# Kernel tuning notes

Measured on AMD Instinct MI355X. Metric: run time of the kernel, lower is better.

## Reference

```python
import jax, jax.numpy as jnp
import numpy as np

DIM = 768
H = 12          # num query heads
KV = 6          # num kv heads
GS = H // KV    # group size = 2
HD = DIM // H   # head dim = 64


def setup_inputs() -> dict:
    key = jax.random.key(0)
    ks = jax.random.split(key, 6)
    B, P = 8, 1024
    s = DIM ** -0.5
    x = jax.random.normal(ks[0], (B, P, DIM), dtype=jnp.float32)
    Wq = jax.random.normal(ks[1], (DIM, DIM), dtype=jnp.float32) * s
    Wk = jax.random.normal(ks[2], (DIM, KV * HD), dtype=jnp.float32) * s
    Wv = jax.random.normal(ks[3], (DIM, KV * HD), dtype=jnp.float32) * s
    Wp = jax.random.normal(ks[4], (DIM, DIM), dtype=jnp.float32) * s
    bp = jnp.zeros((DIM,), dtype=jnp.float32)
    return {"x": x, "Wq": Wq, "Wk": Wk, "Wv": Wv, "Wp": Wp, "bp": bp}


def reference(x, Wq, Wk, Wv, Wp, bp):
    B, P, C = x.shape
    scale = HD ** -0.5
    # projections; consecutive heads i*GS..(i+1)*GS-1 form kv-group i (torch.split dim=1)
    q = (x @ Wq).reshape(B, P, KV, GS, HD).transpose(0, 2, 3, 1, 4) * scale  # [B,KV,GS,P,d]
    k = (x @ Wk).reshape(B, P, KV, HD).transpose(0, 2, 1, 3)                 # [B,KV,P,d]
    v = (x @ Wv).reshape(B, P, KV, HD).transpose(0, 2, 1, 3)                 # [B,KV,P,d]

    scores = jnp.einsum('bghqd,bgkd->bghqk', q, k)      # [B,KV,GS,P,P]
    w = jax.nn.softmax(scores, axis=-1)                  # attn_drop=0 (eval)
    att = jnp.einsum('bghqk,bgkd->bghqd', w, v)          # [B,KV,GS,P,d]

    # per-group row-matched gaussian-ish noise (torch get_gaussian), vectorized over KV groups
    y = P * HD
    flat = att.reshape(B, KV, GS, y)                     # rows = groups within kv-group
    M = jax.random.uniform(jax.random.key(42), (KV, GS, y), dtype=flat.dtype)
    di = jnp.arange(min(GS, y))
    M = M.at[:, di, di].set(0.0)                         # sparse: zero diagonal
    m_mean = M.mean(axis=-1, keepdims=True)
    m_std = jnp.std(M, axis=-1, ddof=1, keepdims=True)   # torch.std is unbiased
    m_std = jnp.where(m_std == 0, jnp.ones_like(m_std), m_std)
    Z = (M - m_mean) / m_std                             # [KV,GS,y], shared across batch
    r_mean = flat.mean(axis=-1, keepdims=True)           # [B,KV,GS,1]
    r_std = jnp.std(flat, axis=-1, ddof=1, keepdims=True)
    flat = flat - (Z[None] * r_std + r_mean)

    att = flat.reshape(B, KV, GS, P, HD).reshape(B, H, P, HD)
    out = att.transpose(0, 2, 1, 3).reshape(B, P, C) @ Wp + bp  # proj_drop=0
    return out
```

## Files before the change

kernel.cpp:

```cpp
#include <hip/hip_runtime.h>
#include <hip/hip_bf16.h>
#include <math.h>


#define NTHREADS 256

typedef __bf16 bf16x8 __attribute__((ext_vector_type(8)));
typedef float f32x4 __attribute__((ext_vector_type(4)));

#define MFMA16(a, b, c) __builtin_amdgcn_mfma_f32_16x16x32_bf16(a, b, c, 0, 0, 0)

#define QSCALE 0.18033688011112042f

__device__ __forceinline__ float fexp2(float x) {
#if __has_builtin(__builtin_amdgcn_exp2f)
    return __builtin_amdgcn_exp2f(x);
#else
    return __expf(x * 0.6931471805599453f);
#endif
}

__device__ __forceinline__ void gload16(const void* g, void* l) {
    __builtin_amdgcn_global_load_lds(
        (const __attribute__((address_space(1))) void*)g,
        (__attribute__((address_space(3))) void*)l, 16, 0, 0);
}

__device__ __forceinline__ unsigned rotl_u32(unsigned x, int r) {
    return (x << r) | (x >> (32 - r));
}
__device__ __forceinline__ void threefry_0_42(unsigned x0, unsigned x1,
                                              unsigned& o0, unsigned& o1) {
    const unsigned ks0 = 0u, ks1 = 42u, ks2 = 0u ^ 42u ^ 0x1BD11BDAu;
    x0 += ks0; x1 += ks1;
#define R4(a,b,c,d) \
    x0 += x1; x1 = rotl_u32(x1,a); x1 ^= x0; \
    x0 += x1; x1 = rotl_u32(x1,b); x1 ^= x0; \
    x0 += x1; x1 = rotl_u32(x1,c); x1 ^= x0; \
    x0 += x1; x1 = rotl_u32(x1,d); x1 ^= x0;
    R4(13,15,26,6)   x0 += ks1; x1 += ks2 + 1u;
    R4(17,29,16,24)  x0 += ks2; x1 += ks0 + 2u;
    R4(13,15,26,6)   x0 += ks0; x1 += ks1 + 3u;
    R4(17,29,16,24)  x0 += ks1; x1 += ks2 + 4u;
    R4(13,15,26,6)   x0 += ks2; x1 += ks0 + 5u;
#undef R4
    o0 = x0; o1 = x1;
}
__device__ __forceinline__ float tf_uniform(unsigned i) {
    unsigned o0, o1;
    threefry_0_42(0u, i, o0, o1);
    unsigned bits = o0 ^ o1;
    return __uint_as_float((bits >> 9) | 0x3f800000u) - 1.0f;
}

__device__ __forceinline__ float wave_sum64(float v) {
#pragma unroll
    for (int off = 32; off; off >>= 1) v += __shfl_xor(v, off, 64);
    return v;
}

__device__ __forceinline__ unsigned short bf16_rne(float x) {
    unsigned u = __float_as_uint(x);
    return (unsigned short)((u + 0x7fffu + ((u >> 16) & 1u)) >> 16);
}
__device__ __forceinline__ unsigned pack_bf16x2(float lo, float hi) {
    unsigned ul = __float_as_uint(lo), uh = __float_as_uint(hi);
    unsigned rl = ul + 0x7fffu + ((ul >> 16) & 1u);
    unsigned rh = uh + 0x7fffu + ((uh >> 16) & 1u);
    return __builtin_amdgcn_perm(rh, rl, 0x07060302u);
}
__device__ __forceinline__ float bfu(unsigned v) {
    return __uint_as_float(v << 16);
}


__global__ __launch_bounds__(NTHREADS) void prep_k(
    const float* __restrict__ x, const float* __restrict__ Wq,
    const float* __restrict__ Wk, const float* __restrict__ Wv,
    const float* __restrict__ Wp,
    unsigned short* __restrict__ xb, unsigned short* __restrict__ wstk,
    unsigned short* __restrict__ wpt,
    unsigned short* __restrict__ zb, float* __restrict__ zpart)
{
    __shared__ float rbuf[8];
    int blk = blockIdx.x;
    if (blk < 1536) {
#pragma unroll
        for (int j = 0; j < 4; ++j) {
            int i = blk * 1024 + j * 256 + threadIdx.x;
            float4 v = ((const float4*)x)[i];
            uint2 u;
            u.x = pack_bf16x2(v.x, v.y);
            u.y = pack_bf16x2(v.z, v.w);
            int f0 = i * 4;
            int row = f0 / 768, col = f0 - row * 768;
            int kc = col >> 6, kin = col & 63;
            int kh = kin >> 5, g = (kin >> 3) & 3, e = col & 7;
            int chunk = row >> 4, cl = row & 15;
            size_t a = (((size_t)(kc * 512 + chunk)) * 2 + kh) * 512
                       + (g * 16 + cl) * 8 + e;
            *(uint2*)&xb[a] = u;
        }
    } else if (blk < 1920) {
        int zc = blk - 1536;
        int row = zc >> 5, chunk = zc & 31;
        int g = row & 1;
        int j0 = chunk * 2048;
        float sum = 0.f, sumsq = 0.f;
        for (int t = threadIdx.x; t < 2048; t += NTHREADS) {
            int j = j0 + t;
            unsigned i = (unsigned)row * 65536u + (unsigned)j;
            float m = tf_uniform(i);
            if (j == g) m = 0.f;
            zb[i] = bf16_rne(m);
            sum += m; sumsq += m * m;
        }
        sum = wave_sum64(sum); sumsq = wave_sum64(sumsq);
        int lane = threadIdx.x & 63, wv = threadIdx.x >> 6;
        if (lane == 0) { rbuf[wv] = sum; rbuf[4 + wv] = sumsq; }
        __syncthreads();
        if (threadIdx.x == 0) {
            zpart[zc * 2]     = rbuf[0] + rbuf[1] + rbuf[2] + rbuf[3];
            zpart[zc * 2 + 1] = rbuf[4] + rbuf[5] + rbuf[6] + rbuf[7];
        }
    } else {
        int id = blk - 1920;
        const float* W; unsigned short* dstbuf; int N, rowbase, NC;
        if (id < 144)      { W = Wq; dstbuf = wstk; N = 768; rowbase = 0;    NC = 96; }
        else if (id < 216) { W = Wk; dstbuf = wstk; N = 384; rowbase = 768;  NC = 96; id -= 144; }
        else if (id < 288) { W = Wv; dstbuf = wstk; N = 384; rowbase = 1152; NC = 96; id -= 216; }
        else               { W = Wp; dstbuf = wpt;  N = 768; rowbase = 0;    NC = 48; id -= 288; }
        int ntn = N >> 6;
        int kt = id / ntn, nt = id % ntn;
        int k0 = kt * 64, n0 = nt * 64;
        int t = threadIdx.x;
        int tn = t & 63, tk = t >> 6;
        float r[16];
#pragma unroll
        for (int j = 0; j < 16; ++j)
            r[j] = W[(size_t)(k0 + tk * 16 + j) * N + n0 + tn];
        uint4 u0, u1;
        u0.x = pack_bf16x2(r[0], r[1]);   u0.y = pack_bf16x2(r[2], r[3]);
        u0.z = pack_bf16x2(r[4], r[5]);   u0.w = pack_bf16x2(r[6], r[7]);
        u1.x = pack_bf16x2(r[8], r[9]);   u1.y = pack_bf16x2(r[10], r[11]);
        u1.z = pack_bf16x2(r[12], r[13]); u1.w = pack_bf16x2(r[14], r[15]);
        int rowg = rowbase + n0 + tn;
        int chunk = rowg >> 4, cl = rowg & 15;
        int kc = k0 >> 6;
        int kh = tk >> 1, g0 = (tk & 1) * 2;
        size_t base = (((size_t)(kc * NC + chunk)) * 2 + kh) * 512 + cl * 8;
        *(uint4*)&dstbuf[base + g0 * 128]       = u0;
        *(uint4*)&dstbuf[base + (g0 + 1) * 128] = u1;
    }
}

__device__ __forceinline__ void mfma_tile128x256(
    const unsigned short* __restrict__ Afb, int nca,
    const unsigned short* __restrict__ Bfb,
    int row0, int col0,
    unsigned short* As, unsigned short* Bs, f32x4 acc[4][4])
{
    const int tid = threadIdx.x;
    const int lane = tid & 63, w = tid >> 6;
    const int c = lane & 15, g = lane >> 4;
    const int wm = w & 1, wn = w >> 1;

#pragma unroll
    for (int mi = 0; mi < 4; ++mi)
#pragma unroll
        for (int ni = 0; ni < 4; ++ni) acc[mi][ni] = (f32x4){0.f, 0.f, 0.f, 0.f};

    const unsigned short* Abase = Afb + (size_t)(row0 >> 4) * 1024;
    const unsigned short* Bbase = Bfb + (size_t)(col0 >> 4) * 1024;

    for (int kc = 0; kc < 12; ++kc) {
        const unsigned short* a = Abase + (size_t)kc * nca * 1024;
        const unsigned short* bb = Bbase + (size_t)kc * 512 * 1024;
        __syncthreads();
        gload16(a  + tid * 8,         As + tid * 8);
        gload16(a  + tid * 8 + 4096,  As + tid * 8 + 4096);
        gload16(bb + tid * 8,         Bs + tid * 8);
        gload16(bb + tid * 8 + 4096,  Bs + tid * 8 + 4096);
        gload16(bb + tid * 8 + 8192,  Bs + tid * 8 + 8192);
        gload16(bb + tid * 8 + 12288, Bs + tid * 8 + 12288);
        __syncthreads();
#pragma unroll
        for (int ks = 0; ks < 2; ++ks) {
            bf16x8 aA[4], bB[4];
#pragma unroll
            for (int mi = 0; mi < 4; ++mi)
                aA[mi] = *(const bf16x8*)&As[(wm * 4 + mi) * 1024 + ks * 512 + g * 128 + c * 8];
#pragma unroll
            for (int ni = 0; ni < 4; ++ni)
                bB[ni] = *(const bf16x8*)&Bs[(wn * 4 + ni) * 1024 + ks * 512 + g * 128 + c * 8];
#pragma unroll
            for (int mi = 0; mi < 4; ++mi)
#pragma unroll
                for (int ni = 0; ni < 4; ++ni)
                    acc[mi][ni] = MFMA16(aA[mi], bB[ni], acc[mi][ni]);
        }
    }
}

__global__ __launch_bounds__(512) void qkv_mfma_k(
    const unsigned short* __restrict__ xb, const unsigned short* __restrict__ wstk,
    unsigned short* __restrict__ qbh, unsigned short* __restrict__ kb2,
    unsigned short* __restrict__ vb2)
{
    __shared__ unsigned short As[8192];
    __shared__ unsigned short Bs[16384];
    int id = blockIdx.x;
    int xcd = id & 7, slot = id >> 3;
    int col0i = xcd + ((slot & 3) << 3);
    int row0i = slot >> 2;
    int row0 = row0i * 128, col0 = col0i * 256;
    f32x4 acc[4][4];
    mfma_tile128x256(wstk, 96, xb, row0, col0, As, Bs, acc);

    const int tid = threadIdx.x;
    const int w = tid >> 6, lane = tid & 63;
    const int c = lane & 15, g = lane >> 4;
    const int wm = w & 1, wn = w >> 1;

#pragma unroll
    for (int mi = 0; mi < 4; ++mi) {
        int ocb = row0 + wm * 64 + mi * 16;
        int ocol = ocb + g * 4;
#pragma unroll
        for (int ni = 0; ni < 4; ++ni) {
            int pglob = col0 + wn * 64 + ni * 16 + c;
            int b = pglob >> 10, pin = pglob & 1023;
            if (ocb < 768) {
                ushort4 u;
                u.x = bf16_rne(acc[mi][ni][0] * QSCALE);
                u.y = bf16_rne(acc[mi][ni][1] * QSCALE);
                u.z = bf16_rne(acc[mi][ni][2] * QSCALE);
                u.w = bf16_rne(acc[mi][ni][3] * QSCALE);
                int h = ocol >> 6, d0 = ocol & 63;
                *(ushort4*)&qbh[(((size_t)b * 12 + h) * 1024 + pin) * 64 + d0] = u;
            } else if (ocb < 1152) {
                int kcol = ocol - 768;
                int kv = kcol >> 6, d0 = kcol & 63;
                int kt = pin >> 7, key = pin & 127;
                ushort4 u;
                u.x = bf16_rne(acc[mi][ni][0]);
                u.y = bf16_rne(acc[mi][ni][1]);
                u.z = bf16_rne(acc[mi][ni][2]);
                u.w = bf16_rne(acc[mi][ni][3]);
                *(ushort4*)&kb2[((((size_t)(b * 6 + kv) * 8 + kt) * 8 + (d0 >> 3)) * 128
                                 + key) * 8 + (d0 & 7)] = u;
            } else {
                int kt = pin >> 7, pg = (pin & 127) >> 3, p8 = pin & 7;
#pragma unroll
                for (int r = 0; r < 4; ++r) {
                    int vcol = ocol + r - 1152;
                    int kv = vcol >> 6, d = vcol & 63;
                    vb2[((((size_t)(b * 6 + kv) * 8 + kt) * 16 + pg) * 64 + d) * 8 + p8]
                        = bf16_rne(acc[mi][ni][r]);
                }
            }
        }
    }
}

__global__ __launch_bounds__(512) void proj_mfma_k(
    const unsigned short* __restrict__ attb, const unsigned short* __restrict__ wpt,
    const float* __restrict__ bp, float* __restrict__ out)
{
    __shared__ unsigned short As[8192];
    __shared__ unsigned short Bs[16384];
    int id = blockIdx.x;
    int xcd = id & 7, slot = id >> 3;
    int col0i = xcd + ((slot & 3) << 3);
    int row0i = slot >> 2;
    int row0 = row0i * 128, col0 = col0i * 256;
    f32x4 acc[4][4];
    mfma_tile128x256(wpt, 48, attb, row0, col0, As, Bs, acc);

    const int tid = threadIdx.x;
    const int w = tid >> 6, lane = tid & 63;
    const int c = lane & 15, g = lane >> 4;
    const int wm = w & 1, wn = w >> 1;
#pragma unroll
    for (int mi = 0; mi < 4; ++mi) {
        int ocol = row0 + wm * 64 + mi * 16 + g * 4;
        float4 bias = *(const float4*)&bp[ocol];
#pragma unroll
        for (int ni = 0; ni < 4; ++ni) {
            int p = col0 + wn * 64 + ni * 16 + c;
            float4 u;
            u.x = acc[mi][ni][0] + bias.x;
            u.y = acc[mi][ni][1] + bias.y;
            u.z = acc[mi][ni][2] + bias.z;
            u.w = acc[mi][ni][3] + bias.w;
            *(float4*)&out[(size_t)p * 768 + ocol] = u;
        }
    }
}

#define LDP 140
__global__ __launch_bounds__(NTHREADS) void attn_mfma_k(
    const unsigned short* __restrict__ qbh, const unsigned short* __restrict__ kb2,
    const unsigned short* __restrict__ vb2, unsigned short* __restrict__ attb,
    float* __restrict__ spart)
{
    __shared__ unsigned short Ks[8192];
    __shared__ unsigned short Vs[8192];
    __shared__ unsigned short P_lds[4 * 16 * LDP];
    __shared__ float l_s[4][32];
    __shared__ float sbuf[8];

    int id = blockIdx.x;
    int xcd = id & 7, slot = id >> 3;
    int grp = slot % 6, member = slot / 6;
    int g48 = xcd + 8 * grp;
    int b = g48 / 6, kv = g48 % 6;
    int h = kv * 2 + (member & 1);
    int qtile = member >> 1;
    const int qt0 = qtile * 128;

    const int tid = threadIdx.x;
    const int w = tid >> 6, lane = tid & 63;
    const int c = lane & 15, g = lane >> 4;

    const unsigned short* qh = qbh + (((size_t)b * 12 + h) * 1024 + qt0 + w * 32) * 64;
    const unsigned short* kbase = kb2 + ((size_t)(b * 6 + kv) * 8) * 8192;
    const unsigned short* vbase = vb2 + ((size_t)(b * 6 + kv) * 8) * 8192;
    unsigned short* Pw = P_lds + w * 16 * LDP;

    bf16x8 bQ[2][2];
#pragma unroll
    for (int ks = 0; ks < 2; ++ks) {
        bQ[ks][0] = *(const bf16x8*)(qh + (size_t)(c) * 64 + ks * 32 + g * 8);
        bQ[ks][1] = *(const bf16x8*)(qh + (size_t)(16 + c) * 64 + ks * 32 + g * 8);
    }

    f32x4 O[2][4];
#pragma unroll
    for (int i = 0; i < 2; ++i)
#pragma unroll
        for (int j = 0; j < 4; ++j) O[i][j] = (f32x4){0.f, 0.f, 0.f, 0.f};
    float l_r[2] = {0.f, 0.f};

    for (int t = 0; t < 8; ++t) {
        const unsigned short* kt = kbase + (size_t)t * 8192;
        const unsigned short* vt = vbase + (size_t)t * 8192;

        __syncthreads();
        gload16(kt + tid * 8,        Ks + tid * 8);
        gload16(kt + tid * 8 + 2048, Ks + tid * 8 + 2048);
        gload16(kt + tid * 8 + 4096, Ks + tid * 8 + 4096);
        gload16(kt + tid * 8 + 6144, Ks + tid * 8 + 6144);
        gload16(vt + tid * 8,        Vs + tid * 8);
        gload16(vt + tid * 8 + 2048, Vs + tid * 8 + 2048);
        gload16(vt + tid * 8 + 4096, Vs + tid * 8 + 4096);
        gload16(vt + tid * 8 + 6144, Vs + tid * 8 + 6144);
        __syncthreads();

        f32x4 S[8][2];
#pragma unroll
        for (int mb = 0; mb < 8; ++mb) {
            S[mb][0] = (f32x4){0.f, 0.f, 0.f, 0.f};
            S[mb][1] = (f32x4){0.f, 0.f, 0.f, 0.f};
        }
#pragma unroll
        for (int ks = 0; ks < 2; ++ks)
#pragma unroll
            for (int mb = 0; mb < 8; ++mb) {
                bf16x8 aK = *(const bf16x8*)&Ks[((ks * 4 + g) * 128 + mb * 16 + c) * 8];
                S[mb][0] = MFMA16(aK, bQ[ks][0], S[mb][0]);
                S[mb][1] = MFMA16(aK, bQ[ks][1], S[mb][1]);
            }

#pragma unroll
        for (int qn = 0; qn < 2; ++qn) {
            float lt = 0.f;
#pragma unroll
            for (int mb = 0; mb < 8; ++mb) {
                float p0 = fexp2(S[mb][qn][0]);
                float p1 = fexp2(S[mb][qn][1]);
                float p2 = fexp2(S[mb][qn][2]);
                float p3 = fexp2(S[mb][qn][3]);
                lt += (p0 + p1) + (p2 + p3);
                uint2 uu;
                uu.x = pack_bf16x2(p0, p1);
                uu.y = pack_bf16x2(p2, p3);
                *(uint2*)&Pw[(size_t)c * LDP + mb * 16 + g * 4] = uu;
            }
            lt += __shfl_xor(lt, 16, 64);
            lt += __shfl_xor(lt, 32, 64);
            l_r[qn] += lt;
#pragma unroll
            for (int ks = 0; ks < 4; ++ks) {
                bf16x8 aP = *(const bf16x8*)&Pw[(size_t)c * LDP + ks * 32 + g * 8];
#pragma unroll
                for (int nb = 0; nb < 4; ++nb) {
                    bf16x8 bV = *(const bf16x8*)&Vs[((ks * 4 + g) * 64 + nb * 16 + c) * 8];
                    O[qn][nb] = MFMA16(aP, bV, O[qn][nb]);
                }
            }
        }
    }
    if (g == 0) { l_s[w][c] = l_r[0]; l_s[w][16 + c] = l_r[1]; }
    f32x4 li0 = *(f32x4*)&l_s[w][g * 4];
    f32x4 li1 = *(f32x4*)&l_s[w][16 + g * 4];
    float inv0[4], inv1[4];
#pragma unroll
    for (int r = 0; r < 4; ++r) { inv0[r] = 1.f / li0[r]; inv1[r] = 1.f / li1[r]; }
    int rowblk = (b * 1024 + qt0 + w * 32) >> 4;
    float psum = 0.f, psumsq = 0.f;
#pragma unroll
    for (int r = 0; r < 4; ++r) {
        int cl = g * 4 + r;
#pragma unroll
        for (int nb = 0; nb < 4; ++nb) {
            float o0 = O[0][nb][r] * inv0[r];
            float o1 = O[1][nb][r] * inv1[r];
            psum += o0 + o1;
            psumsq += o0 * o0 + o1 * o1;
            int kh = nb >> 1, gb = (nb & 1) * 2 + (c >> 3), e = c & 7;
            size_t a0 = (((size_t)h * 512 + rowblk) * 2 + kh) * 512
                        + (gb * 16 + cl) * 8 + e;
            size_t a1 = (((size_t)h * 512 + rowblk + 1) * 2 + kh) * 512
                        + (gb * 16 + cl) * 8 + e;
            attb[a0] = bf16_rne(o0);
            attb[a1] = bf16_rne(o1);
        }
    }
    psum = wave_sum64(psum); psumsq = wave_sum64(psumsq);
    if (lane == 0) { sbuf[w] = psum; sbuf[4 + w] = psumsq; }
    __syncthreads();
    if (tid == 0) {
        int idx = ((b * 12 + h) * 8 + qtile) * 2;
        spart[idx]     = sbuf[0] + sbuf[1] + sbuf[2] + sbuf[3];
        spart[idx + 1] = sbuf[4] + sbuf[5] + sbuf[6] + sbuf[7];
    }
}

__global__ __launch_bounds__(NTHREADS) void stats2_k(
    unsigned short* __restrict__ attb, const unsigned short* __restrict__ zb,
    const float* __restrict__ spart, const float* __restrict__ zpart)
{
    int blk = blockIdx.x;
    int bh = blk >> 3, ch = blk & 7;
    int b = bh / 12, h = bh % 12;
    float zs = 0.f, zs2 = 0.f, rs = 0.f, rs2 = 0.f;
#pragma unroll
    for (int cc = 0; cc < 32; ++cc) {
        zs  += zpart[(h * 32 + cc) * 2];
        zs2 += zpart[(h * 32 + cc) * 2 + 1];
    }
#pragma unroll
    for (int cc = 0; cc < 8; ++cc) {
        rs  += spart[(bh * 8 + cc) * 2];
        rs2 += spart[(bh * 8 + cc) * 2 + 1];
    }
    float m_mean = zs * (1.f / 65536.f);
    float m_var  = (zs2 - 65536.f * m_mean * m_mean) * (1.f / 65535.f);
    float m_sd   = sqrtf(fmaxf(m_var, 0.f));
    if (m_sd == 0.f) m_sd = 1.f;
    float r_mean = rs * (1.f / 65536.f);
    float r_var  = (rs2 - 65536.f * r_mean * r_mean) * (1.f / 65535.f);
    float r_sd   = sqrtf(fmaxf(r_var, 0.f));
    float a = r_sd / m_sd;
    float bc = m_mean * a - r_mean;

    const unsigned short* zrow = zb + (size_t)h * 65536 + (size_t)ch * 8192;
    for (int f = threadIdx.x; f < 1024; f += NTHREADS) {
        int p = f >> 3, dq = (f & 7) * 8;
        int row = b * 1024 + ch * 128 + p;
        int chunk = row >> 4, cl = row & 15;
        int kh = dq >> 5, gb = (dq >> 3) & 3;
        size_t aoff = (((size_t)h * 512 + chunk) * 2 + kh) * 512 + (gb * 16 + cl) * 8;
        unsigned short* ptr = attb + aoff;
        uint4 u = *(const uint4*)ptr;
        uint4 zu = *(const uint4*)(zrow + (size_t)f * 8);
        float v0 = bfu(u.x)       - bfu(zu.x)       * a + bc;
        float v1 = bfu(u.x >> 16) - bfu(zu.x >> 16) * a + bc;
        float v2 = bfu(u.y)       - bfu(zu.y)       * a + bc;
        float v3 = bfu(u.y >> 16) - bfu(zu.y >> 16) * a + bc;
        float v4 = bfu(u.z)       - bfu(zu.z)       * a + bc;
        float v5 = bfu(u.z >> 16) - bfu(zu.z >> 16) * a + bc;
        float v6 = bfu(u.w)       - bfu(zu.w)       * a + bc;
        float v7 = bfu(u.w >> 16) - bfu(zu.w >> 16) * a + bc;
        uint4 o;
        o.x = pack_bf16x2(v0, v1);
        o.y = pack_bf16x2(v2, v3);
        o.z = pack_bf16x2(v4, v5);
        o.w = pack_bf16x2(v6, v7);
        *(uint4*)ptr = o;
    }
}

extern "C" void kernel_launch(void* const* d_in, const int* in_sizes, int n_in,
                              void* d_out, int out_size, void* d_ws, size_t ws_size,
                              hipStream_t stream) {
    const float* x  = (const float*)d_in[0];
    const float* Wq = (const float*)d_in[1];
    const float* Wk = (const float*)d_in[2];
    const float* Wv = (const float*)d_in[3];
    const float* Wp = (const float*)d_in[4];
    const float* bp = (const float*)d_in[5];
    float* out = (float*)d_out;

    float* ws    = (float*)d_ws;
    float* zpart = ws;
    float* spart = zpart + 768;
    unsigned short* zb   = (unsigned short*)(spart + 1536);
    unsigned short* xb   = zb + 786432;
    unsigned short* wstk = xb + 6291456;
    unsigned short* wpt  = wstk + 1179648;
    unsigned short* qbh  = wpt + 589824;
    unsigned short* kb2  = qbh + 6291456;
    unsigned short* vb2  = kb2 + 3145728;
    unsigned short* attb = vb2 + 3145728;

    prep_k<<<2352, NTHREADS, 0, stream>>>(x, Wq, Wk, Wv, Wp,
                                          xb, wstk, wpt, zb, zpart);
    qkv_mfma_k<<<384, 512, 0, stream>>>(xb, wstk, qbh, kb2, vb2);
    attn_mfma_k<<<768, NTHREADS, 0, stream>>>(qbh, kb2, vb2, attb, spart);
    stats2_k<<<768, NTHREADS, 0, stream>>>(attb, zb, spart, zpart);
    proj_mfma_k<<<192, 512, 0, stream>>>(attb, wpt, bp, out);
}
```

Baseline: 218.9 us.

## Merge GQA head pair into one 512-thread attention block with double-buffered K/V

The attention kernel now launches 384 blocks of 512 threads, with the two query heads that share a KV group handled by one block, so each K/V tile is staged once for both heads. K/V tiles are double-buffered in LDS and prefetched two iterations ahead using vmcnt waits and raw barriers, overlapping global-to-LDS loads with MFMA work. The aim is to halve K/V global traffic and hide load latency. In exchange, LDS use per block roughly doubles and there are fewer blocks, which may lower occupancy.

```diff
diff --git a/kernel.cpp b/kernel.cpp
--- a/kernel.cpp
+++ b/kernel.cpp
@@ -299,31 +299,32 @@
 }
 
 #define LDP 140
-__global__ __launch_bounds__(NTHREADS) void attn_mfma_k(
+__global__ __launch_bounds__(512) void attn_mfma_k(
     const unsigned short* __restrict__ qbh, const unsigned short* __restrict__ kb2,
     const unsigned short* __restrict__ vb2, unsigned short* __restrict__ attb,
     float* __restrict__ spart)
 {
-    __shared__ unsigned short Ks[8192];
-    __shared__ unsigned short Vs[8192];
-    __shared__ unsigned short P_lds[4 * 16 * LDP];
-    __shared__ float l_s[4][32];
-    __shared__ float sbuf[8];
+    __shared__ unsigned short Ks[2][8192];
+    __shared__ unsigned short Vs[2][8192];
+    __shared__ unsigned short P_lds[8 * 16 * LDP];
+    __shared__ float l_s[8][32];
+    __shared__ float sbuf[16];
 
     int id = blockIdx.x;
     int xcd = id & 7, slot = id >> 3;
-    int grp = slot % 6, member = slot / 6;
+    int grp = slot % 6, qtile = slot / 6;
     int g48 = xcd + 8 * grp;
     int b = g48 / 6, kv = g48 % 6;
-    int h = kv * 2 + (member & 1);
-    int qtile = member >> 1;
     const int qt0 = qtile * 128;
 
     const int tid = threadIdx.x;
     const int w = tid >> 6, lane = tid & 63;
     const int c = lane & 15, g = lane >> 4;
-
-    const unsigned short* qh = qbh + (((size_t)b * 12 + h) * 1024 + qt0 + w * 32) * 64;
+    const int hh = w >> 2;
+    const int h = kv * 2 + hh;
+    const int qsub = w & 3;
+
+    const unsigned short* qh = qbh + (((size_t)b * 12 + h) * 1024 + qt0 + qsub * 32) * 64;
     const unsigned short* kbase = kb2 + ((size_t)(b * 6 + kv) * 8) * 8192;
     const unsigned short* vbase = vb2 + ((size_t)(b * 6 + kv) * 8) * 8192;
     unsigned short* Pw = P_lds + w * 16 * LDP;
@@ -342,20 +343,24 @@
         for (int j = 0; j < 4; ++j) O[i][j] = (f32x4){0.f, 0.f, 0.f, 0.f};
     float l_r[2] = {0.f, 0.f};
 
+#define STAGE_KV(t, bi) do {                                                  \
+        const unsigned short* kt_ = kbase + (size_t)(t) * 8192;               \
+        const unsigned short* vt_ = vbase + (size_t)(t) * 8192;               \
+        gload16(kt_ + tid * 8,        &Ks[bi][tid * 8]);                      \
+        gload16(kt_ + tid * 8 + 4096, &Ks[bi][tid * 8 + 4096]);               \
+        gload16(vt_ + tid * 8,        &Vs[bi][tid * 8]);                      \
+        gload16(vt_ + tid * 8 + 4096, &Vs[bi][tid * 8 + 4096]);               \
+    } while (0)
+
+    STAGE_KV(0, 0);
+    STAGE_KV(1, 1);
+
+#pragma unroll 1
     for (int t = 0; t < 8; ++t) {
-        const unsigned short* kt = kbase + (size_t)t * 8192;
-        const unsigned short* vt = vbase + (size_t)t * 8192;
-
-        __syncthreads();
-        gload16(kt + tid * 8,        Ks + tid * 8);
-        gload16(kt + tid * 8 + 2048, Ks + tid * 8 + 2048);
-        gload16(kt + tid * 8 + 4096, Ks + tid * 8 + 4096);
-        gload16(kt + tid * 8 + 6144, Ks + tid * 8 + 6144);
-        gload16(vt + tid * 8,        Vs + tid * 8);
-        gload16(vt + tid * 8 + 2048, Vs + tid * 8 + 2048);
-        gload16(vt + tid * 8 + 4096, Vs + tid * 8 + 4096);
-        gload16(vt + tid * 8 + 6144, Vs + tid * 8 + 6144);
-        __syncthreads();
+        const int bi = t & 1;
+        if (t < 7) { asm volatile("s_waitcnt vmcnt(4)" ::: "memory"); }
+        else       { asm volatile("s_waitcnt vmcnt(0)" ::: "memory"); }
+        __builtin_amdgcn_s_barrier();
 
         f32x4 S[8][2];
 #pragma unroll
@@ -367,7 +372,7 @@
         for (int ks = 0; ks < 2; ++ks)
 #pragma unroll
             for (int mb = 0; mb < 8; ++mb) {
-                bf16x8 aK = *(const bf16x8*)&Ks[((ks * 4 + g) * 128 + mb * 16 + c) * 8];
+                bf16x8 aK = *(const bf16x8*)&Ks[bi][((ks * 4 + g) * 128 + mb * 16 + c) * 8];
                 S[mb][0] = MFMA16(aK, bQ[ks][0], S[mb][0]);
                 S[mb][1] = MFMA16(aK, bQ[ks][1], S[mb][1]);
             }
@@ -395,19 +400,24 @@
                 bf16x8 aP = *(const bf16x8*)&Pw[(size_t)c * LDP + ks * 32 + g * 8];
 #pragma unroll
                 for (int nb = 0; nb < 4; ++nb) {
-                    bf16x8 bV = *(const bf16x8*)&Vs[((ks * 4 + g) * 64 + nb * 16 + c) * 8];
+                    bf16x8 bV = *(const bf16x8*)&Vs[bi][((ks * 4 + g) * 64 + nb * 16 + c) * 8];
                     O[qn][nb] = MFMA16(aP, bV, O[qn][nb]);
                 }
             }
         }
-    }
+
+        __builtin_amdgcn_s_barrier();
+        if (t + 2 < 8) STAGE_KV(t + 2, bi);
+    }
+#undef STAGE_KV
+
     if (g == 0) { l_s[w][c] = l_r[0]; l_s[w][16 + c] = l_r[1]; }
     f32x4 li0 = *(f32x4*)&l_s[w][g * 4];
     f32x4 li1 = *(f32x4*)&l_s[w][16 + g * 4];
     float inv0[4], inv1[4];
 #pragma unroll
     for (int r = 0; r < 4; ++r) { inv0[r] = 1.f / li0[r]; inv1[r] = 1.f / li1[r]; }
-    int rowblk = (b * 1024 + qt0 + w * 32) >> 4;
+    int rowblk = (b * 1024 + qt0 + qsub * 32) >> 4;
     float psum = 0.f, psumsq = 0.f;
 #pragma unroll
     for (int r = 0; r < 4; ++r) {
@@ -428,12 +438,15 @@
         }
     }
     psum = wave_sum64(psum); psumsq = wave_sum64(psumsq);
-    if (lane == 0) { sbuf[w] = psum; sbuf[4 + w] = psumsq; }
+    if (lane == 0) { sbuf[w] = psum; sbuf[8 + w] = psumsq; }
     __syncthreads();
     if (tid == 0) {
-        int idx = ((b * 12 + h) * 8 + qtile) * 2;
-        spart[idx]     = sbuf[0] + sbuf[1] + sbuf[2] + sbuf[3];
-        spart[idx + 1] = sbuf[4] + sbuf[5] + sbuf[6] + sbuf[7];
+        int i0 = ((b * 12 + kv * 2) * 8 + qtile) * 2;
+        spart[i0]     = sbuf[0] + sbuf[1] + sbuf[2] + sbuf[3];
+        spart[i0 + 1] = sbuf[8] + sbuf[9] + sbuf[10] + sbuf[11];
+        int i1 = ((b * 12 + kv * 2 + 1) * 8 + qtile) * 2;
+        spart[i1]     = sbuf[4] + sbuf[5] + sbuf[6] + sbuf[7];
+        spart[i1 + 1] = sbuf[12] + sbuf[13] + sbuf[14] + sbuf[15];
     }
 }
 
@@ -518,7 +531,7 @@
     prep_k<<<2352, NTHREADS, 0, stream>>>(x, Wq, Wk, Wv, Wp,
                                           xb, wstk, wpt, zb, zpart);
     qkv_mfma_k<<<384, 512, 0, stream>>>(xb, wstk, qbh, kb2, vb2);
-    attn_mfma_k<<<768, NTHREADS, 0, stream>>>(qbh, kb2, vb2, attb, spart);
+    attn_mfma_k<<<384, 512, 0, stream>>>(qbh, kb2, vb2, attb, spart);
     stats2_k<<<768, NTHREADS, 0, stream>>>(attb, zb, spart, zpart);
     proj_mfma_k<<<192, 512, 0, stream>>>(attb, wpt, bp, out);
 }
```

After: 214.8 us. No clear change (-1.9%).
